# Kernel tuning notes

Hardware: AMD Instinct MI355X
Metric: run time of the kernel (lower is better)

Reference implementation:

```python
import jax, jax.numpy as jnp
import numpy as np

E = 21   # numParticipants (experts)
D = 128  # input features (hardcoded Linear(128,16))
H = 16   # hidden
N = 262144  # rows


def setup_inputs() -> dict:
    key = jax.random.key(0)
    ks = jax.random.split(key, 6)
    x = jax.random.normal(ks[0], (N, D), dtype=jnp.float32)
    sid = jax.random.randint(ks[1], (N,), 0, E)
    s1 = 1.0 / np.sqrt(D)
    W1 = jax.random.uniform(ks[2], (E, D, H), jnp.float32, -s1, s1)
    b1 = jax.random.uniform(ks[3], (E, H), jnp.float32, -s1, s1)
    s2 = 1.0 / np.sqrt(H)
    W2 = jax.random.uniform(ks[4], (E, H), jnp.float32, -s2, s2)  # Linear(16,1) weight, squeezed
    b2 = jax.random.uniform(ks[5], (E,), jnp.float32, -s2, s2)
    return {"x": x, "sid": sid, "W1": W1, "b1": b1, "W2": W2, "b2": b2}


def reference(x, sid, W1, b1, W2, b2):
    # Per-row expert MLP: h = relu(x @ W1[sid] + b1[sid]); y = relu(h . W2[sid] + b2[sid]).
    # Dropout(0.5) is identity in eval mode. Vectorized routing: compute first layer for
    # all 21 tiny experts ([N,E,H] ~ 350MB), then select the routed expert per row.
    h_all = jax.nn.relu(jnp.einsum('nd,edh->neh', x, W1) + b1[None, :, :])  # [N,E,H]
    h = jnp.take_along_axis(h_all, sid[:, None, None], axis=1)[:, 0, :]      # [N,H]
    y = jax.nn.relu(jnp.einsum('nh,nh->n', h, W2[sid]) + b2[sid])            # [N]
    return y[:, None]  # [N,1]
```

## Files before the change

### kernel.cpp

```cpp
#include <hip/hip_runtime.h>
#include <stdint.h>

#define N_ROWS 262144
#define DIM    128
#define HID    16
#define NEXP   21
#define NSEG   (N_ROWS / 64 + NEXP)
#define NBLK1  256
#define RPB    (N_ROWS / NBLK1)
#define RPT    (RPB / 256)

#define PADB     1040
#define WAVE_LDS (8 * PADB)
#define BLK_LDS  (4 * WAVE_LDS)

__global__ __launch_bounds__(256) void k_hist(const int* __restrict__ sid,
                                              int* __restrict__ counts,
                                              int* __restrict__ blockBase) {
    __shared__ int lh[NEXP];
    int t = threadIdx.x;
    if (t < NEXP) lh[t] = 0;
    __syncthreads();
    int base = blockIdx.x * RPB + t;
#pragma unroll
    for (int r = 0; r < RPT; r++) {
        atomicAdd(&lh[sid[base + r * 256]], 1);
    }
    __syncthreads();
    if (t < NEXP) blockBase[blockIdx.x * NEXP + t] = atomicAdd(&counts[t], lh[t]);
}

__global__ __launch_bounds__(256) void k_scatter(const int* __restrict__ sid,
                                                 const int* __restrict__ counts,
                                                 const int* __restrict__ blockBase,
                                                 int* __restrict__ buckets) {
    __shared__ int sbase[NEXP];
    __shared__ int lcur[NEXP];
    int t = threadIdx.x;
    if (t == 0) {
        int acc = 0;
        for (int e = 0; e < NEXP; e++) {
            sbase[e] = acc + blockBase[blockIdx.x * NEXP + e];
            acc += ((counts[e] + 63) >> 6) << 6;
        }
    }
    if (t < NEXP) lcur[t] = 0;
    __syncthreads();
    int base = blockIdx.x * RPB + t;
#pragma unroll
    for (int r = 0; r < RPT; r++) {
        int row = base + r * 256;
        int e = sid[row];
        int lp = atomicAdd(&lcur[e], 1);
        buckets[sbase[e] + lp] = row | (e << 24);
    }
}

typedef __attribute__((address_space(1))) const uint32_t gu32;
typedef __attribute__((address_space(3))) uint32_t lu32;

__device__ __forceinline__ void stage16(const float* gp, char* lp) {
    __builtin_amdgcn_global_load_lds((gu32*)(uintptr_t)gp,
                                     (lu32*)(uintptr_t)lp, 16, 0, 0);
}

__device__ __forceinline__ float bcast(float v, int lane) {
    return __uint_as_float(__builtin_amdgcn_readlane(__float_as_uint(v), lane));
}

__global__ __launch_bounds__(256, 4) void k_main4(const float* __restrict__ x,
                                                  const float* __restrict__ W1,
                                                  const float* __restrict__ b1,
                                                  const float* __restrict__ W2,
                                                  const float* __restrict__ b2,
                                                  const int* __restrict__ buckets,
                                                  float* __restrict__ out) {
    extern __shared__ char smem[];
    const int seg = blockIdx.x * 4 + (threadIdx.x >> 6);
    if (seg >= NSEG) return;
    const int lane = threadIdx.x & 63;
    char* waveLds = smem + (threadIdx.x >> 6) * WAVE_LDS;

    int ent = buckets[seg * 64 + lane];
    if (__ballot(ent >= 0) == 0ULL) return;
    const int e = __builtin_amdgcn_readfirstlane(ent) >> 24;
    const int row = ent & 0x00FFFFFF;
    const int vrow = (ent >= 0) ? row : 0;

    int rg[8];
#pragma unroll
    for (int g = 0; g < 8; g++) rg[g] = __shfl(vrow, g * 8 + (lane >> 3), 64);
    const int c8 = lane & 7;

    const float* __restrict__ w1 = W1 + e * (DIM * HID);
    float h[HID];
#pragma unroll
    for (int j = 0; j < HID; j++) h[j] = b1[e * HID + j];

    const char* rb = waveLds + (lane >> 3) * PADB + (lane & 7) * 128;

#pragma unroll 1
    for (int q = 0; q < 4; q++) {
        __builtin_amdgcn_s_waitcnt(0);
#pragma unroll
        for (int g = 0; g < 8; g++) {
            const float* gp = x + (size_t)rg[g] * DIM + q * 32 + c8 * 4;
            stage16(gp, waveLds + g * PADB + lane * 16);
        }
        const float* __restrict__ w1q = w1 + q * 512;
        float wq[8];
#pragma unroll
        for (int m = 0; m < 8; m++) wq[m] = w1q[m * 64 + lane];
        __builtin_amdgcn_s_waitcnt(0);
#pragma unroll
        for (int m = 0; m < 8; m++) {
            const float4 xv = *(const float4*)(rb + m * 16);
            const float xc[4] = {xv.x, xv.y, xv.z, xv.w};
#pragma unroll
            for (int c = 0; c < 4; c++) {
#pragma unroll
                for (int j = 0; j < HID; j++)
                    h[j] = fmaf(xc[c], bcast(wq[m], c * 16 + j), h[j]);
            }
        }
    }

    float acc = b2[e];
#pragma unroll
    for (int j = 0; j < HID; j++) acc = fmaf(fmaxf(h[j], 0.0f), W2[e * HID + j], acc);
    if (ent >= 0) out[row] = fmaxf(acc, 0.0f);
}

__global__ __launch_bounds__(256) void k_naive(const float* __restrict__ x,
                                               const int* __restrict__ sid,
                                               const float* __restrict__ W1,
                                               const float* __restrict__ b1,
                                               const float* __restrict__ W2,
                                               const float* __restrict__ b2,
                                               float* __restrict__ out) {
    int row = blockIdx.x * 256 + threadIdx.x;
    if (row >= N_ROWS) return;
    int e = sid[row];
    const float* w1 = W1 + e * (DIM * HID);
    const float* xr = x + (size_t)row * DIM;
    float h[HID];
#pragma unroll
    for (int j = 0; j < HID; j++) h[j] = b1[e * HID + j];
    for (int k = 0; k < DIM; k++) {
        float xk = xr[k];
#pragma unroll
        for (int j = 0; j < HID; j++) h[j] = fmaf(xk, w1[k * HID + j], h[j]);
    }
    float acc = b2[e];
#pragma unroll
    for (int j = 0; j < HID; j++) acc = fmaf(fmaxf(h[j], 0.0f), W2[e * HID + j], acc);
    out[row] = fmaxf(acc, 0.0f);
}

extern "C" void kernel_launch(void* const* d_in, const int* in_sizes, int n_in,
                              void* d_out, int out_size, void* d_ws, size_t ws_size,
                              hipStream_t stream) {
    const float* x   = (const float*)d_in[0];
    const int*   sid = (const int*)d_in[1];
    const float* W1  = (const float*)d_in[2];
    const float* b1  = (const float*)d_in[3];
    const float* W2  = (const float*)d_in[4];
    const float* b2  = (const float*)d_in[5];
    float* out = (float*)d_out;

    const size_t bucketBytes = (size_t)NSEG * 64 * sizeof(int);
    const size_t countBytes  = 32 * sizeof(int);
    const size_t bbBytes     = (size_t)NBLK1 * NEXP * sizeof(int);
    const size_t need = bucketBytes + countBytes + bbBytes;

    if (ws_size < need) {
        k_naive<<<(N_ROWS + 255) / 256, 256, 0, stream>>>(x, sid, W1, b1, W2, b2, out);
        return;
    }

    char* ws = (char*)d_ws;
    int* buckets   = (int*)ws;
    int* counts    = (int*)(ws + bucketBytes);
    int* blockBase = (int*)(ws + bucketBytes + countBytes);

    hipMemsetAsync(buckets, 0xFF, bucketBytes, stream);
    hipMemsetAsync(counts, 0, countBytes, stream);
    k_hist<<<NBLK1, 256, 0, stream>>>(sid, counts, blockBase);
    k_scatter<<<NBLK1, 256, 0, stream>>>(sid, counts, blockBase, buckets);
    k_main4<<<(NSEG + 3) / 4, 256, BLK_LDS, stream>>>(x, W1, b1, W2, b2, buckets, out);
}
```

Baseline: 221.3 us.

## Stage full 64-row x tile into XOR-swizzled LDS in one-wave blocks

The main kernel now runs one wave per block and copies the whole 64x128 x tile into 32 KB of LDS up front with a single wait. Before, it staged four 32-column slices, each followed by a full wait. Each lane reads its own row's data through an XOR swizzle to avoid bank conflicts. The goal is more loads in flight per wave and fewer serialized waits on memory, at the cost of more LDS per wave and possibly lower occupancy per CU.

```diff
diff --git a/kernel.cpp b/kernel.cpp
--- a/kernel.cpp
+++ b/kernel.cpp
@@ -10,9 +10,7 @@
 #define RPB    (N_ROWS / NBLK1)
 #define RPT    (RPB / 256)
 
-#define PADB     1040
-#define WAVE_LDS (8 * PADB)
-#define BLK_LDS  (4 * WAVE_LDS)
+#define BLK_LDS  (64 * 512)
 
 __global__ __launch_bounds__(256) void k_hist(const int* __restrict__ sid,
                                               int* __restrict__ counts,
@@ -64,63 +62,63 @@
                                      (lu32*)(uintptr_t)lp, 16, 0, 0);
 }
 
-__device__ __forceinline__ float bcast(float v, int lane) {
-    return __uint_as_float(__builtin_amdgcn_readlane(__float_as_uint(v), lane));
+__device__ __forceinline__ float bcast(float v, int srclane) {
+    return __uint_as_float(__builtin_amdgcn_readlane(__float_as_uint(v), srclane));
 }
 
-__global__ __launch_bounds__(256, 4) void k_main4(const float* __restrict__ x,
-                                                  const float* __restrict__ W1,
-                                                  const float* __restrict__ b1,
-                                                  const float* __restrict__ W2,
-                                                  const float* __restrict__ b2,
-                                                  const int* __restrict__ buckets,
-                                                  float* __restrict__ out) {
-    extern __shared__ char smem[];
-    const int seg = blockIdx.x * 4 + (threadIdx.x >> 6);
-    if (seg >= NSEG) return;
-    const int lane = threadIdx.x & 63;
-    char* waveLds = smem + (threadIdx.x >> 6) * WAVE_LDS;
-
+__global__ __launch_bounds__(64, 1) void k_main6(const float* __restrict__ x,
+                                                 const float* __restrict__ W1,
+                                                 const float* __restrict__ b1,
+                                                 const float* __restrict__ W2,
+                                                 const float* __restrict__ b2,
+                                                 const int* __restrict__ buckets,
+                                                 float* __restrict__ out) {
+    __shared__ char lds[BLK_LDS];
+    const int seg = blockIdx.x;
+    const int lane = threadIdx.x;
     int ent = buckets[seg * 64 + lane];
     if (__ballot(ent >= 0) == 0ULL) return;
     const int e = __builtin_amdgcn_readfirstlane(ent) >> 24;
     const int row = ent & 0x00FFFFFF;
     const int vrow = (ent >= 0) ? row : 0;
 
-    int rg[8];
+    const int half = lane >> 5;
+    const int c32 = lane & 31;
 #pragma unroll
-    for (int g = 0; g < 8; g++) rg[g] = __shfl(vrow, g * 8 + (lane >> 3), 64);
-    const int c8 = lane & 7;
+    for (int p = 0; p < 32; p++) {
+        const int slot = 2 * p + half;
+        const int rowp = __shfl(vrow, slot, 64);
+        const int chunk = c32 ^ (slot & 31);
+        const float* gp = x + (size_t)(unsigned)rowp * DIM + chunk * 4;
+        stage16(gp, lds + p * 1024 + lane * 16);
+    }
 
-    const float* __restrict__ w1 = W1 + e * (DIM * HID);
     float h[HID];
 #pragma unroll
     for (int j = 0; j < HID; j++) h[j] = b1[e * HID + j];
 
-    const char* rb = waveLds + (lane >> 3) * PADB + (lane & 7) * 128;
+    __builtin_amdgcn_s_waitcnt(0);
+
+    const float* __restrict__ w1 = W1 + e * (DIM * HID);
+    const char* rowbase = lds + lane * 512;
+    const int sL = lane & 31;
 
 #pragma unroll 1
     for (int q = 0; q < 4; q++) {
-        __builtin_amdgcn_s_waitcnt(0);
-#pragma unroll
-        for (int g = 0; g < 8; g++) {
-            const float* gp = x + (size_t)rg[g] * DIM + q * 32 + c8 * 4;
-            stage16(gp, waveLds + g * PADB + lane * 16);
-        }
         const float* __restrict__ w1q = w1 + q * 512;
         float wq[8];
 #pragma unroll
         for (int m = 0; m < 8; m++) wq[m] = w1q[m * 64 + lane];
-        __builtin_amdgcn_s_waitcnt(0);
 #pragma unroll
         for (int m = 0; m < 8; m++) {
-            const float4 xv = *(const float4*)(rb + m * 16);
+            const int c = q * 8 + m;
+            const float4 xv = *(const float4*)(rowbase + (((c ^ sL) & 31) << 4));
             const float xc[4] = {xv.x, xv.y, xv.z, xv.w};
 #pragma unroll
-            for (int c = 0; c < 4; c++) {
+            for (int t = 0; t < 4; t++) {
 #pragma unroll
                 for (int j = 0; j < HID; j++)
-                    h[j] = fmaf(xc[c], bcast(wq[m], c * 16 + j), h[j]);
+                    h[j] = fmaf(xc[t], bcast(wq[m], t * 16 + j), h[j]);
             }
         }
     }
@@ -187,5 +185,5 @@
     hipMemsetAsync(counts, 0, countBytes, stream);
     k_hist<<<NBLK1, 256, 0, stream>>>(sid, counts, blockBase);
     k_scatter<<<NBLK1, 256, 0, stream>>>(sid, counts, blockBase, buckets);
-    k_main4<<<(NSEG + 3) / 4, 256, BLK_LDS, stream>>>(x, W1, b1, W2, b2, buckets, out);
+    k_main6<<<NSEG, 64, 0, stream>>>(x, W1, b1, W2, b2, buckets, out);
 }
```

Result: slower. 240.6 us (+8.7%).
